# Optimization experiments

Measured on AMD Instinct MI355X. Metric: run time of the kernel, lower is better.

## Reference

```python
import jax, jax.numpy as jnp
import numpy as np
from jax import lax

K = 3          # kernel (patch size)
D = 64         # MPO bond dimension
F = K * K      # feature dim per patch (k^2 * C, C=1)
S = F          # output-index spacing inside each SMPO
OUT = 10       # final output dimension
B = 128        # batch size
H = 81         # image height = width
SIGMA = 1e-3   # 'random_eye' noise scale


def patch_embed(x, k=K):
    """squeeze_image + trigonometric embedding.
    x: (B, h, w) -> unit vectors (B, N, 2) with N=(h/k)*(w/k).
    Each k*k patch row is embedded as the L2-normalized mean of
    [cos(pi/2 x), sin(pi/2 x)] over its k^2 features."""
    b, h, w = x.shape
    p = x.reshape(b, h // k, k, w // k, k).transpose(0, 1, 3, 2, 4)
    p = p.reshape(b, (h // k) * (w // k), k * k)
    ang = 0.5 * jnp.pi * p
    v = jnp.stack([jnp.cos(ang).mean(-1), jnp.sin(ang).mean(-1)], axis=-1)
    return v / jnp.linalg.norm(v, axis=-1, keepdims=True)


def smpo_layer(v, W_out, W_mid):
    """Spaced MPO applied to a product-state MPS, read out per output site.
    v:      (B, n, 2)  input site vectors (n = J*S sites, output at every S-th)
    W_out:  (J, D, D, 2, F)  output-site tensors (identity baseline baked in)
    W_mid:  (J, S-1, D, D, 2) non-output site tensors; effective matrix is
            M = I + einsum('bp,dep->bde', v, W) ('random_eye' init).
    Output row j = L_j . A_j(v) . R_j where L/R are left/right chain
    environments with the other output indices closed with ones.
    Returns (B, J, F)."""
    b, n, _ = v.shape
    J = W_out.shape[0]
    s = n // J
    eye = jnp.eye(D, dtype=v.dtype)
    vg = v.reshape(b, J, s, 2)
    v_out = vg[:, :, 0, :].transpose(1, 0, 2)        # (J, B, 2)
    v_mid = vg[:, :, 1:, :].transpose(1, 2, 0, 3)    # (J, S-1, B, 2)

    def left_step(l, xs):
        A, vo, Wm, vm = xs
        Lj = l                                       # env left of output site j
        l = jnp.einsum('bd,bp,depf->be', l, vo, A)   # Abar (f summed = ones closure)
        for t in range(s - 1):
            M = eye + jnp.einsum('bp,dep->bde', vm[t], Wm[t])
            l = jnp.einsum('bd,bde->be', l, M)
        return l, Lj

    def right_step(r, xs):
        A, vo, Wm, vm = xs
        for t in reversed(range(s - 1)):
            M = eye + jnp.einsum('bp,dep->bde', vm[t], Wm[t])
            r = jnp.einsum('bde,be->bd', M, r)
        Rj = r                                       # env right of output site j
        r = jnp.einsum('bp,depf,be->bd', vo, A, r)
        return r, Rj

    bnd = jnp.zeros((b, D), v.dtype).at[:, 0].set(1.0)  # bond-1 boundary
    xs = (W_out, v_out, W_mid, v_mid)
    _, L = lax.scan(jax.checkpoint(left_step), bnd, xs)
    _, R = lax.scan(jax.checkpoint(right_step), bnd, xs, reverse=True)
    return jnp.einsum('jbd,jdepf,jbp,jbe->bjf', L, W_out, v_out, R)


def final_layer(x, A0, W_mid):
    """Final SMPO (spacing = n, single output index at site 0), fully
    contracted left-to-right. x: (B, n) -> (B, OUT)."""
    ang = 0.5 * jnp.pi * x
    v = jnp.stack([jnp.cos(ang), jnp.sin(ang)], axis=-1)   # (B, n, 2)
    eye = jnp.eye(D, dtype=x.dtype)
    u = jnp.einsum('bp,epo->beo', v[:, 0], A0[0])          # left boundary e0

    def step(u, xs):
        Wm, vm = xs
        M = eye + jnp.einsum('bp,dep->bde', vm, Wm)
        return jnp.einsum('bdo,bde->beo', u, M), None

    u, _ = lax.scan(jax.checkpoint(step), u, (W_mid, v[:, 1:].transpose(1, 0, 2)))
    return u[:, 0, :]                                      # right boundary e0


def setup_inputs() -> dict:
    key = jax.random.key(0)
    ks = jax.random.split(key, 7)
    eyeD = np.eye(D, dtype=np.float32)

    def wout(k, J):  # identity baseline + noise ('random_eye')
        base = jnp.asarray((0.8 / F) * eyeD[:, :, None, None])
        return base + SIGMA * jax.random.normal(k, (J, D, D, 2, F), jnp.float32)

    def wmid(k, J):
        return SIGMA * jax.random.normal(k, (J, S - 1, D, D, 2), jnp.float32)

    x = jax.random.uniform(ks[0], (B, H, H, 1), jnp.float32)
    Wout0 = wout(ks[1], 81)
    Wmid0 = wmid(ks[2], 81)
    Wout1 = wout(ks[3], 9)
    Wmid1 = wmid(ks[4], 9)
    A0f = jnp.asarray(0.1 * eyeD[:, :, None, None]) + SIGMA * jax.random.normal(
        ks[5], (D, D, 2, OUT), jnp.float32)
    WmidF = SIGMA * jax.random.normal(ks[6], (80, D, D, 2), jnp.float32)
    return {"x": x, "Wout0": Wout0, "Wmid0": Wmid0, "Wout1": Wout1,
            "Wmid1": Wmid1, "A0f": A0f, "WmidF": WmidF}


def reference(x, Wout0, Wmid0, Wout1, Wmid1, A0f, WmidF):
    v0 = patch_embed(x[..., 0])                    # (B, 729, 2)
    h1 = smpo_layer(v0, Wout0, Wmid0)              # (B, 81, 9)
    v1 = patch_embed(h1.reshape(-1, 27, 27))       # (B, 81, 2)
    h2 = smpo_layer(v1, Wout1, Wmid1)              # (B, 9, 9)
    return final_layer(h2.reshape(-1, 81), A0f, WmidF)  # (B, 10)
```

## Files before the change

kernel.cpp:

```cpp
#include <hip/hip_runtime.h>
#include <cstdint>
#include <cstddef>


typedef float    f32x16 __attribute__((ext_vector_type(16)));
typedef _Float16 f16x8  __attribute__((ext_vector_type(8)));
typedef __fp16   fp16x2 __attribute__((ext_vector_type(2)));
typedef _Float16 h2_t   __attribute__((ext_vector_type(2)));
typedef const void __attribute__((address_space(1))) gas_t;
typedef void       __attribute__((address_space(3))) las_t;

union U16  { uint4 u; f16x8 h; };
union B16u { uint32_t u[4]; f16x8 h; };
union H2U  { fp16x2 h; uint32_t u; };

__device__ __forceinline__ uint32_t pkf16(float a, float b){
  H2U z; z.h = __builtin_amdgcn_cvt_pkrtz(a, b); return z.u;
}
__device__ __forceinline__ uint32_t pkmul(uint32_t a, uint32_t b){
  H2U x, y, r; x.u = a; y.u = b;
  r.h = x.h * y.h; return r.u;
}
__device__ __forceinline__ uint32_t packh2(float a, float b){
  union { _Float16 h[2]; uint32_t u; } z;
  z.h[0] = (_Float16)a; z.h[1] = (_Float16)b; return z.u;
}
__device__ __forceinline__ float fdot2f(uint32_t wa, uint32_t wb, float acc){
  union U { uint32_t u; h2_t h; };
  U a, b; a.u = wa; b.u = wb;
  return __builtin_amdgcn_fdot2(a.h, b.h, acc, false);
}

#define REC 17408

__global__ void k_build(const float* __restrict__ Wmid, const float* __restrict__ Wout,
                        char* __restrict__ S, int J, int n, int dirR){
  int tid = blockIdx.x*256 + threadIdx.x;
  if (tid >= n*4096) return;
  int gt = tid >> 12, r = tid & 4095;
  int f = r >> 8, ln = (r >> 2) & 63, dw = r & 3;
  int s = f >> 1, m = f & 1;
  int row = m*32 + (ln & 31);
  int kb = s*16 + (ln >> 5)*8 + dw*2;
  int p = kb >> 6, q = kb & 63;
  int jj = gt/9, pos = gt - jj*9;
  int j = dirR ? (J-1-jj) : jj;
  int outs = dirR ? 8 : 0;
  float w[2];
  #pragma unroll
  for (int k2 = 0; k2 < 2; ++k2){
    int qq = q + k2;
    int d = dirR ? row : qq;
    int e = dirR ? qq : row;
    float val;
    if (pos == outs){
      const float* src = Wout + ((((size_t)j*64 + d)*64 + e)*2 + p)*9;
      val = 0.f;
      #pragma unroll
      for (int ff = 0; ff < 9; ++ff) val += src[ff];
      if (d == e) val -= 0.8f;
    } else {
      int mi = dirR ? (7 - pos) : (pos - 1);
      val = Wmid[((((size_t)j*8 + mi)*64 + d)*64 + e)*2 + p];
    }
    w[k2] = val;
  }
  uint32_t* S32 = (uint32_t*)(S + (size_t)gt*REC);
  S32[f*256 + ln*4 + dw] = packh2(w[0]*256.f, w[1]*256.f);
}

__global__ void k_buildF(const float* __restrict__ Wm, char* __restrict__ S){
  int tid = blockIdx.x*256 + threadIdx.x;
  if (tid >= 80*4096) return;
  int gt = tid >> 12, r = tid & 4095;
  int f = r >> 8, ln = (r >> 2) & 63, dw = r & 3;
  int s = f >> 1, m = f & 1;
  int row = m*32 + (ln & 31);
  int kb = s*16 + (ln >> 5)*8 + dw*2;
  int p = kb >> 6, q = kb & 63;
  float w[2];
  #pragma unroll
  for (int k2 = 0; k2 < 2; ++k2){
    int d = q + k2, e = row;
    w[k2] = Wm[(((size_t)gt*64 + d)*64 + e)*2 + p];
  }
  uint32_t* S32 = (uint32_t*)(S + (size_t)gt*REC);
  S32[f*256 + ln*4 + dw] = packh2(w[0]*256.f, w[1]*256.f);
}

__global__ void k_vrec(const float2* __restrict__ v, char* __restrict__ S,
                       int n, int nv, int mode){
  int tid = blockIdx.x*256 + threadIdx.x;
  if (tid >= n*128) return;
  int gt = tid >> 7, b = tid & 127;
  int site = (mode == 0) ? gt : (mode == 1) ? (n-1-gt) : (gt+1);
  *(float2*)(S + (size_t)gt*REC + 16384 + b*8) = v[(size_t)b*nv + site];
}

__global__ void k_embed(const float* __restrict__ img, int Wd, int PG,
                        float2* __restrict__ outv){
  int tid = blockIdx.x*256 + threadIdx.x;
  int NP = PG*PG;
  if (tid >= 128*NP) return;
  int b = tid / NP, s = tid - b*NP;
  int pi = s / PG, pj = s - pi*PG;
  const float* base = img + (size_t)b*Wd*Wd + (size_t)(3*pi)*Wd + 3*pj;
  float cs = 0.f, sn = 0.f;
  #pragma unroll
  for (int r = 0; r < 3; ++r){
    #pragma unroll
    for (int c = 0; c < 3; ++c){
      float x = base[r*Wd + c];
      float s_, c_; sincosf(1.5707963267948966f*x, &s_, &c_);
      cs += c_; sn += s_;
    }
  }
  cs *= (1.f/9.f); sn *= (1.f/9.f);
  float rn = rsqrtf(cs*cs + sn*sn);
  float2 v; v.x = cs*rn; v.y = sn*rn;
  outv[tid] = v;
}

__device__ __forceinline__ void stage17(const char* g, char* l){
  #pragma unroll
  for (int i = 0; i < 17; ++i)
    __builtin_amdgcn_global_load_lds((gas_t*)(const void*)(g + i*1024),
                                     (las_t*)(void*)(l + i*1024), 16, 0, 0);
}

#define MKBASE(acc, bd) do { \
  uint32_t P0 = pkf16(acc[0],acc[1]),  P1 = pkf16(acc[2],acc[3]); \
  uint32_t P2 = pkf16(acc[4],acc[5]),  P3 = pkf16(acc[6],acc[7]); \
  uint32_t Q0 = (uint32_t)__shfl_xor((int)P0, 32); \
  uint32_t Q1 = (uint32_t)__shfl_xor((int)P1, 32); \
  uint32_t Q2 = (uint32_t)__shfl_xor((int)P2, 32); \
  uint32_t Q3 = (uint32_t)__shfl_xor((int)P3, 32); \
  bd[0] = hlo ? P0 : Q2;  bd[1] = hlo ? P1 : Q3; \
  bd[2] = hlo ? Q0 : P2;  bd[3] = hlo ? Q1 : P3; \
  uint32_t R0 = pkf16(acc[8],acc[9]),   R1 = pkf16(acc[10],acc[11]); \
  uint32_t R2 = pkf16(acc[12],acc[13]), R3 = pkf16(acc[14],acc[15]); \
  uint32_t T0 = (uint32_t)__shfl_xor((int)R0, 32); \
  uint32_t T1 = (uint32_t)__shfl_xor((int)R1, 32); \
  uint32_t T2 = (uint32_t)__shfl_xor((int)R2, 32); \
  uint32_t T3 = (uint32_t)__shfl_xor((int)R3, 32); \
  bd[4] = hlo ? R0 : T2;  bd[5] = hlo ? R1 : T3; \
  bd[6] = hlo ? T0 : R2;  bd[7] = hlo ? T1 : R3; \
} while(0)

#define MFMA8(slotp) do { \
  const uint4* fr_ = (const uint4*)(slotp); \
  _Pragma("unroll") \
  for (int s_ = 0; s_ < 8; ++s_){ \
    const int sl_ = s_ & 3; \
    const uint32_t* bb_ = (sl_ < 2) ? bd0 : bd1; \
    const int off_ = (sl_ & 1)*4; \
    const uint32_t scl_ = (s_ < 4) ? px : py; \
    B16u bs_; \
    _Pragma("unroll") \
    for (int dw_ = 0; dw_ < 4; ++dw_) bs_.u[dw_] = pkmul(bb_[off_+dw_], scl_); \
    U16 fa0_, fa1_; \
    fa0_.u = fr_[(2*s_)*64 + ln]; \
    fa1_.u = fr_[(2*s_+1)*64 + ln]; \
    acc0 = __builtin_amdgcn_mfma_f32_32x32x16_f16(fa0_.h, bs_.h, acc0, 0, 0, 0); \
    acc1 = __builtin_amdgcn_mfma_f32_32x32x16_f16(fa1_.h, bs_.h, acc1, 0, 0, 0); \
  } \
} while(0)

#define PROD_SLOOP(buf) do { \
  const uint4* fr = (const uint4*)(buf); \
  _Pragma("unroll") \
  for (int s = 0; s < 8; ++s){ \
    const int sl = s & 3; \
    const uint32_t scl = (s < 4) ? px : py; \
    const int off = (sl & 1)*4; \
    U16 f0, f1; \
    f0.u = fr[(2*s)*64 + ln]; \
    f1.u = fr[(2*s+1)*64 + ln]; \
    { \
      const uint32_t* bb = (sl < 2) ? bl0 : bh0; \
      B16u bs; \
      _Pragma("unroll") \
      for (int dw = 0; dw < 4; ++dw) bs.u[dw] = pkmul(bb[off+dw], scl); \
      a00 = __builtin_amdgcn_mfma_f32_32x32x16_f16(f0.h, bs.h, a00, 0, 0, 0); \
      a10 = __builtin_amdgcn_mfma_f32_32x32x16_f16(f1.h, bs.h, a10, 0, 0, 0); \
    } \
    { \
      const uint32_t* bb = (sl < 2) ? bl1 : bh1; \
      B16u bs; \
      _Pragma("unroll") \
      for (int dw = 0; dw < 4; ++dw) bs.u[dw] = pkmul(bb[off+dw], scl); \
      a01 = __builtin_amdgcn_mfma_f32_32x32x16_f16(f0.h, bs.h, a01, 0, 0, 0); \
      a11 = __builtin_amdgcn_mfma_f32_32x32x16_f16(f1.h, bs.h, a11, 0, 0, 0); \
    } \
  } \
} while(0)

#define PROD_INIT_I() do { \
  _Pragma("unroll") \
  for (int i = 0; i < 16; ++i){ a00[i]=0.f; a01[i]=0.f; a10[i]=0.f; a11[i]=0.f; } \
  if (((i32 >> 2) & 1) == h){ \
    int rr0 = (i32 & 3) | ((i32 >> 3) << 2); \
    _Pragma("unroll") \
    for (int rr = 0; rr < 16; ++rr) \
      if (rr == rr0){ a00[rr] = 1.f; a11[rr] = 1.f; } \
  } \
} while(0)

#define PROD_WRITEOUT(ob, diagc) do { \
  _Pragma("unroll") \
  for (int x = 0; x < 2; ++x){ \
    _Pragma("unroll") \
    for (int y = 0; y < 2; ++y){ \
      const f32x16& A = (x==0) ? (y==0 ? a00 : a01) : (y==0 ? a10 : a11); \
      int C = y*32 + i32; \
      _Pragma("unroll") \
      for (int r = 0; r < 16; ++r){ \
        int R = x*32 + (r & 3) + 8*(r >> 2) + 4*h; \
        float val = (A[r] - ((R == C) ? (diagc) : 0.f))*256.f; \
        float oth = __shfl_xor(val, 1); \
        if (!(ln & 1)){ \
          uint32_t dwv = packh2(val, oth); \
          *(uint32_t*)((ob) + R*128 + ((C*2) ^ ((R & 7) << 4))) = dwv; \
        } \
      } \
    } \
  } \
} while(0)

__global__ __launch_bounds__(512, 1) void k_prod(
    const char* __restrict__ sL, const char* __restrict__ sR,
    const float2* __restrict__ v, char* __restrict__ Tn, char* __restrict__ Wn,
    int J){
  __shared__ __align__(16) char lds[3][16384];
  const int ln = threadIdx.x & 63, w = threadIdx.x >> 6;
  const int wid = (blockIdx.x & 7)*(J*4) + (blockIdx.x >> 3);
  const int bg = wid & 15;
  const int pair = wid >> 4;
  const int dir = pair & 1, j = pair >> 1;
  const int b = bg*8 + w;
  const bool hlo = (ln < 32);
  const int h = ln >> 5, i32 = ln & 31;
  const float INV = 1.f/256.f;
  const char* stream = dir ? sR : sL;
  const int n = J*9;

  float2 vv[9];
  {
    const float2* vbase = v + (size_t)b*n + j*9;
    #pragma unroll
    for (int t = 0; t < 9; ++t) vv[t] = vbase[dir ? (9 - t) : t];
  }
  const float alphaC = (dir && j == J-1) ? 1.0f : 0.8f*(vv[0].x + vv[0].y);
  if (dir && j == J-1){ vv[0].x = 0.f; vv[0].y = 0.f; }

  auto gtf = [&](int t) -> int {
    int g = dir ? ((J-2-j)*9 + 8 + t) : (j*9 + t);
    return g < 0 ? 0 : g;
  };
  auto stage = [&](int t, int sl){
    const char* g0 = stream + (size_t)gtf(t)*REC + (size_t)(2*w)*1024 + (size_t)ln*16;
    __builtin_amdgcn_global_load_lds((gas_t*)(const void*)g0,
                                     (las_t*)(void*)(lds[sl] + 2*w*1024), 16, 0, 0);
    __builtin_amdgcn_global_load_lds((gas_t*)(const void*)(g0 + 1024),
                                     (las_t*)(void*)(lds[sl] + (2*w+1)*1024), 16, 0, 0);
  };

  f32x16 a00, a01, a10, a11;
  PROD_INIT_I();

  stage(0, 0);
  stage(1, 1);
  #pragma unroll
  for (int t = 0; t < 9; ++t){
    asm volatile("s_waitcnt vmcnt(2)" ::: "memory");
    __builtin_amdgcn_s_barrier();
    {
      int tn = (t+2 > 8) ? 8 : (t+2);
      stage(tn, (t+2) % 3);
    }
    uint32_t px = pkf16(vv[t].x*INV, vv[t].x*INV);
    uint32_t py = pkf16(vv[t].y*INV, vv[t].y*INV);
    uint32_t bl0[8], bh0[8], bl1[8], bh1[8];
    MKBASE(a00, bl0); MKBASE(a10, bh0);
    MKBASE(a01, bl1); MKBASE(a11, bh1);
    if (t == 0){
      #pragma unroll
      for (int i = 0; i < 16; ++i){
        a00[i] *= alphaC; a01[i] *= alphaC; a10[i] *= alphaC; a11[i] *= alphaC;
      }
    }
    PROD_SLOOP(lds[t % 3]);
  }

  char* ob = (dir ? Wn : Tn) + ((size_t)b*J + j)*8192;
  PROD_WRITEOUT(ob, alphaC);
}

__global__ __launch_bounds__(512, 1) void k_prodF(
    const char* __restrict__ sF, const float2* __restrict__ vF,
    char* __restrict__ GF){
  __shared__ __align__(16) char lds[3][16384];
  const int ln = threadIdx.x & 63, w = threadIdx.x >> 6;
  const int wid = (blockIdx.x & 7)*20 + (blockIdx.x >> 3);
  const int bg = wid & 15, g = wid >> 4;
  const int b = bg*8 + w;
  const bool hlo = (ln < 32);
  const int h = ln >> 5, i32 = ln & 31;
  const float INV = 1.f/256.f;

  float2 vv[8];
  {
    const float2* vbase = vF + (size_t)b*81 + g*8 + 1;
    #pragma unroll
    for (int t = 0; t < 8; ++t) vv[t] = vbase[t];
  }
  auto stage = [&](int t, int sl){
    const char* g0 = sF + (size_t)(g*8 + t)*REC + (size_t)(2*w)*1024 + (size_t)ln*16;
    __builtin_amdgcn_global_load_lds((gas_t*)(const void*)g0,
                                     (las_t*)(void*)(lds[sl] + 2*w*1024), 16, 0, 0);
    __builtin_amdgcn_global_load_lds((gas_t*)(const void*)(g0 + 1024),
                                     (las_t*)(void*)(lds[sl] + (2*w+1)*1024), 16, 0, 0);
  };

  f32x16 a00, a01, a10, a11;
  PROD_INIT_I();

  stage(0, 0);
  stage(1, 1);
  #pragma unroll
  for (int t = 0; t < 8; ++t){
    asm volatile("s_waitcnt vmcnt(2)" ::: "memory");
    __builtin_amdgcn_s_barrier();
    {
      int tn = (t+2 > 7) ? 7 : (t+2);
      stage(tn, (t+2) % 3);
    }
    uint32_t px = pkf16(vv[t].x*INV, vv[t].x*INV);
    uint32_t py = pkf16(vv[t].y*INV, vv[t].y*INV);
    uint32_t bl0[8], bh0[8], bl1[8], bh1[8];
    MKBASE(a00, bl0); MKBASE(a10, bh0);
    MKBASE(a01, bl1); MKBASE(a11, bh1);
    PROD_SLOOP(lds[t % 3]);
  }

  char* ob = GF + ((size_t)b*10 + g)*8192;
  PROD_WRITEOUT(ob, 1.0f);
}

__global__ __launch_bounds__(64, 1) void k_gscan(
    const char* __restrict__ Tn, const char* __restrict__ Wn,
    const float2* __restrict__ v,
    float* __restrict__ Lout, float* __restrict__ Rout, int J){
  __shared__ __align__(16) char slot[4][8192];
  __shared__ __align__(16) float2 vvs[81];
  __shared__ __align__(16) uint32_t pk32[32];
  const int ln = threadIdx.x;
  const int dir = blockIdx.x >> 7;
  const int b = blockIdx.x & 127;
  const float INV = 1.f/256.f;
  const char* P = (dir ? Wn : Tn) + (size_t)b*J*8192;

  for (int g = ln; g < J; g += 64) vvs[g] = v[(size_t)b*(J*9) + (size_t)g*9];

  auto JD = [&](int g){ return dir ? (J-1-g) : g; };
  auto stage8 = [&](int jx, int sl){
    const char* g0 = P + (size_t)jx*8192 + (size_t)ln*16;
    #pragma unroll
    for (int i = 0; i < 8; ++i)
      __builtin_amdgcn_global_load_lds((gas_t*)(const void*)(g0 + i*1024),
                                       (las_t*)(void*)(slot[sl] + i*1024), 16, 0, 0);
  };

  stage8(JD(0), 0);
  stage8(JD(1 < J-1 ? 1 : J-1), 1);
  stage8(JD(2 < J-1 ? 2 : J-1), 2);

  float st = (ln == 0) ? 1.f : 0.f;
  const uint32_t swz = (uint32_t)(ln & 7) << 4;

  #pragma unroll 1
  for (int g = 0; g < J; ++g){
    const int j = JD(g);
    asm volatile("s_waitcnt vmcnt(16)" ::: "memory");
    if (!dir) Lout[((size_t)j*128 + b)*64 + ln] = st;
    {
      int gn = (g+3 > J-1) ? (J-1) : (g+3);
      stage8(JD(gn), (g+3) & 3);
    }

    float c;
    if (dir) c = (j < J-1) ? 0.8f*(vvs[j+1].x + vvs[j+1].y) : 1.0f;
    else     c = 0.8f*(vvs[j].x + vvs[j].y);

    {
      float o = __shfl_xor(st, 1);
      pk32[ln>>1] = (ln & 1) ? packh2(o, st) : packh2(st, o);
    }
    const char* sp = slot[g & 3] + (size_t)ln*128;
    const uint4* lp = (const uint4*)pk32;
    float acc = 0.f;
    #pragma unroll
    for (int m = 0; m < 8; ++m){
      uint4 q = lp[m];
      uint4 ww = *(const uint4*)(sp + ((m*16) ^ swz));
      acc = fdot2f(ww.x, q.x, acc); acc = fdot2f(ww.y, q.y, acc);
      acc = fdot2f(ww.z, q.z, acc); acc = fdot2f(ww.w, q.w, acc);
    }
    st = c*st + acc*INV;
    if (dir) Rout[((size_t)j*128 + b)*64 + ln] = st;
  }
}

__global__ __launch_bounds__(64, 1) void k_fscan(
    const char* __restrict__ GF, const float* __restrict__ A0f,
    const float2* __restrict__ vF, float* __restrict__ outp){
  __shared__ __align__(16) char slot[4][8192];
  __shared__ __align__(16) uint32_t pk[10][32];
  const int ln = threadIdx.x;
  const int b = blockIdx.x;
  const float INV = 1.f/256.f;
  const char* P = GF + (size_t)b*10*8192;

  float2 v0 = vF[(size_t)b*81];
  float u[10];
  #pragma unroll
  for (int o = 0; o < 10; ++o)
    u[o] = v0.x*A0f[(ln*2+0)*10 + o] + v0.y*A0f[(ln*2+1)*10 + o];

  auto stage8 = [&](int g, int sl){
    const char* g0 = P + (size_t)g*8192 + (size_t)ln*16;
    #pragma unroll
    for (int i = 0; i < 8; ++i)
      __builtin_amdgcn_global_load_lds((gas_t*)(const void*)(g0 + i*1024),
                                       (las_t*)(void*)(slot[sl] + i*1024), 16, 0, 0);
  };

  stage8(0, 0);
  stage8(1, 1);
  stage8(2, 2);
  const uint32_t swz = (uint32_t)(ln & 7) << 4;

  #pragma unroll 1
  for (int g = 0; g < 10; ++g){
    asm volatile("s_waitcnt vmcnt(16)" ::: "memory");
    {
      int gn = (g+3 > 9) ? 9 : (g+3);
      stage8(gn, (g+3) & 3);
    }
    #pragma unroll
    for (int o = 0; o < 10; ++o){
      float ot = __shfl_xor(u[o], 1);
      pk[o][ln>>1] = (ln & 1) ? packh2(ot, u[o]) : packh2(u[o], ot);
    }
    const char* sp = slot[g & 3] + (size_t)ln*128;
    uint4 wr[8];
    #pragma unroll
    for (int m = 0; m < 8; ++m) wr[m] = *(const uint4*)(sp + ((m*16) ^ swz));
    #pragma unroll
    for (int o = 0; o < 10; ++o){
      const uint4* lp = (const uint4*)pk[o];
      float acc = 0.f;
      #pragma unroll
      for (int m = 0; m < 8; ++m){
        uint4 q = lp[m];
        acc = fdot2f(wr[m].x, q.x, acc); acc = fdot2f(wr[m].y, q.y, acc);
        acc = fdot2f(wr[m].z, q.z, acc); acc = fdot2f(wr[m].w, q.w, acc);
      }
      u[o] += acc*INV;
    }
  }
  if (ln == 0){
    #pragma unroll
    for (int o = 0; o < 10; ++o) outp[(size_t)b*10 + o] = u[o];
  }
}

__global__ __launch_bounds__(64, 1) void k_scan_m(
    const char* __restrict__ sL, const char* __restrict__ sR,
    float* __restrict__ Lout, float* __restrict__ Rout, int J, int n){
  __shared__ __align__(16) char lds[4*REC];
  const int ln = threadIdx.x;
  const int wg = blockIdx.x;
  const int dir = wg >> 2;
  const int colbase = (wg & 3)*32;
  const char* stream = dir ? sR : sL;
  float* Sout = dir ? Rout : Lout;
  const int outs = dir ? 8 : 0;
  const int b = colbase + (ln & 31);
  const bool hlo = (ln < 32);
  const int h4 = (ln >> 5)*4;
  const float INV = 1.f/256.f;

  f32x16 acc0, acc1;
  #pragma unroll
  for (int i = 0; i < 16; ++i){ acc0[i] = 0.f; acc1[i] = 0.f; }
  if (hlo) acc0[0] = 1.f;

  const char* gsrc = stream + (size_t)ln*16;
  stage17(gsrc,           lds);
  stage17(gsrc + REC,     lds + REC);
  stage17(gsrc + 2*REC,   lds + 2*REC);

  int pos = 0, jj = 0;
  for (int t = 0; t < n; ++t){
    asm volatile("s_waitcnt vmcnt(34)" ::: "memory");
    const char* slot = lds + (size_t)(t & 3)*REC;
    float2 vv = *(const float2*)(slot + 16384 + b*8);
    int tn = t + 3; if (tn > n-1) tn = n-1;
    stage17(gsrc + (size_t)tn*REC, lds + (size_t)(tn & 3)*REC);

    uint32_t px = pkf16(vv.x*INV, vv.x*INV);
    uint32_t py = pkf16(vv.y*INV, vv.y*INV);
    uint32_t bd0[8], bd1[8];
    MKBASE(acc0, bd0);
    MKBASE(acc1, bd1);

    if (pos == outs){
      int jdx = dir ? (J-1-jj) : jj;
      float* dst = Sout + ((size_t)jdx*128 + b)*64;
      #pragma unroll
      for (int q = 0; q < 4; ++q){
        float4 f0; f0.x = acc0[4*q]; f0.y = acc0[4*q+1]; f0.z = acc0[4*q+2]; f0.w = acc0[4*q+3];
        *(float4*)(dst + 8*q + h4) = f0;
        float4 f1; f1.x = acc1[4*q]; f1.y = acc1[4*q+1]; f1.z = acc1[4*q+2]; f1.w = acc1[4*q+3];
        *(float4*)(dst + 32 + 8*q + h4) = f1;
      }
      float alpha = 0.8f*(vv.x + vv.y);
      #pragma unroll
      for (int i = 0; i < 16; ++i){ acc0[i] *= alpha; acc1[i] *= alpha; }
    }

    MFMA8(slot);

    ++pos; if (pos == 9){ pos = 0; ++jj; }
  }
}

__global__ __launch_bounds__(64, 1) void k_final_m(
    const char* __restrict__ sF, const float* __restrict__ A0f,
    const float2* __restrict__ vF, float* __restrict__ outp){
  __shared__ __align__(16) char lds[4*REC];
  const int ln = threadIdx.x;
  const int wg = blockIdx.x;
  const int o = wg >> 2;
  const int b = (wg & 3)*32 + (ln & 31);
  const bool hlo = (ln < 32);
  const int h4 = (ln >> 5)*4;
  const float INV = 1.f/256.f;

  float2 v0 = vF[(size_t)b*81];
  f32x16 acc0, acc1;
  #pragma unroll
  for (int rg = 0; rg < 16; ++rg){
    int row0 = (rg & 3) + 8*(rg >> 2) + h4;
    acc0[rg] = v0.x*A0f[(row0*2+0)*10 + o] + v0.y*A0f[(row0*2+1)*10 + o];
    int row1 = row0 + 32;
    acc1[rg] = v0.x*A0f[(row1*2+0)*10 + o] + v0.y*A0f[(row1*2+1)*10 + o];
  }
  asm volatile("s_waitcnt vmcnt(0)" ::: "memory");

  const char* gsrc = sF + (size_t)ln*16;
  stage17(gsrc,         lds);
  stage17(gsrc + REC,   lds + REC);
  stage17(gsrc + 2*REC, lds + 2*REC);

  const int n = 80;
  for (int t = 0; t < n; ++t){
    asm volatile("s_waitcnt vmcnt(34)" ::: "memory");
    const char* slot = lds + (size_t)(t & 3)*REC;
    float2 vv = *(const float2*)(slot + 16384 + b*8);
    int tn = t + 3; if (tn > n-1) tn = n-1;
    stage17(gsrc + (size_t)tn*REC, lds + (size_t)(tn & 3)*REC);

    uint32_t px = pkf16(vv.x*INV, vv.x*INV);
    uint32_t py = pkf16(vv.y*INV, vv.y*INV);
    uint32_t bd0[8], bd1[8];
    MKBASE(acc0, bd0);
    MKBASE(acc1, bd1);
    MFMA8(slot);
  }
  if (hlo) outp[(size_t)b*10 + o] = acc0[0];
}

template<bool EMB>
__global__ __launch_bounds__(256) void k_out(
    const float* __restrict__ Wout, const float* __restrict__ Lbuf,
    const float* __restrict__ Rbuf, const float2* __restrict__ v, int n,
    float* __restrict__ hout, float2* __restrict__ vF){
  __shared__ float tile[8][64][20];
  __shared__ float Lsh[32][65];
  const int j = blockIdx.x, bh = blockIdx.y;
  const int q = threadIdx.x >> 5, bl = threadIdx.x & 31;
  const int b = bh*32 + bl;
  for (int idx = threadIdx.x; idx < 32*64; idx += 256){
    int r = idx >> 6, d = idx & 63;
    Lsh[r][d] = Lbuf[((size_t)j*128 + bh*32 + r)*64 + d];
  }
  float Rr[8];
  {
    const float4* Rp = (const float4*)(Rbuf + ((size_t)j*128 + b)*64 + q*8);
    ((float4*)Rr)[0] = Rp[0];
    ((float4*)Rr)[1] = Rp[1];
  }
  float acc[18];
  #pragma unroll
  for (int k = 0; k < 18; ++k) acc[k] = 0.f;
  __syncthreads();
  for (int c = 0; c < 8; ++c){
    #pragma unroll
    for (int k = 0; k < 2; ++k){
      int pi = threadIdx.x*2 + k;
      int d8 = pi >> 6, e = pi & 63;
      const float* src = Wout + ((size_t)(j*64 + c*8 + d8)*64 + e)*18;
      float* dst = &tile[d8][e][0];
      #pragma unroll
      for (int mm = 0; mm < 18; ++mm) dst[mm] = src[mm];
    }
    __syncthreads();
    #pragma unroll 1
    for (int d8 = 0; d8 < 8; ++d8){
      float lw = Lsh[bl][c*8 + d8];
      #pragma unroll
      for (int i = 0; i < 8; ++i){
        int e = q*8 + i;
        float wbe = lw * Rr[i];
        const float* tp = &tile[d8][e][0];
        float4 t0 = *(const float4*)(tp);
        float4 t1 = *(const float4*)(tp+4);
        float4 t2 = *(const float4*)(tp+8);
        float4 t3 = *(const float4*)(tp+12);
        float2 t4 = *(const float2*)(tp+16);
        acc[0]  += wbe*t0.x; acc[1]  += wbe*t0.y; acc[2]  += wbe*t0.z; acc[3]  += wbe*t0.w;
        acc[4]  += wbe*t1.x; acc[5]  += wbe*t1.y; acc[6]  += wbe*t1.z; acc[7]  += wbe*t1.w;
        acc[8]  += wbe*t2.x; acc[9]  += wbe*t2.y; acc[10] += wbe*t2.z; acc[11] += wbe*t2.w;
        acc[12] += wbe*t3.x; acc[13] += wbe*t3.y; acc[14] += wbe*t3.z; acc[15] += wbe*t3.w;
        acc[16] += wbe*t4.x; acc[17] += wbe*t4.y;
      }
    }
    __syncthreads();
  }
  float* red = &tile[0][0][0];
  #pragma unroll
  for (int k = 0; k < 18; ++k) red[((size_t)q*32 + bl)*20 + k] = acc[k];
  __syncthreads();
  if (q == 0){
    float s[18];
    #pragma unroll
    for (int k = 0; k < 18; ++k){
      float t = 0.f;
      #pragma unroll
      for (int g = 0; g < 8; ++g) t += red[((size_t)g*32 + bl)*20 + k];
      s[k] = t;
    }
    float2 vo = v[(size_t)b*n + j*9];
    #pragma unroll
    for (int f = 0; f < 9; ++f){
      float val = vo.x*s[f] + vo.y*s[9+f];
      if (EMB){
        float s_, c_; sincosf(1.5707963267948966f*val, &s_, &c_);
        float2 e2; e2.x = c_; e2.y = s_;
        vF[(size_t)b*81 + j*9 + f] = e2;
      } else {
        hout[(size_t)b*729 + j*9 + f] = val;
      }
    }
  }
}

extern "C" void kernel_launch(void* const* d_in, const int* in_sizes, int n_in,
                              void* d_out, int out_size, void* d_ws, size_t ws_size,
                              hipStream_t stream){
  const float* x     = (const float*)d_in[0];
  const float* Wout0 = (const float*)d_in[1];
  const float* Wmid0 = (const float*)d_in[2];
  const float* Wout1 = (const float*)d_in[3];
  const float* Wmid1 = (const float*)d_in[4];
  const float* A0f   = (const float*)d_in[5];
  const float* WmidF = (const float*)d_in[6];
  float* outp = (float*)d_out;

  char* ws = (char*)d_ws;
  size_t off = 0;
  auto alloc = [&](size_t bytes) -> char* {
    char* p = ws + off;
    off = (off + bytes + 255) & ~(size_t)255;
    return p;
  };
  char* S0L = alloc((size_t)729*REC);
  char* S0R = alloc((size_t)729*REC);
  char* S1L = alloc((size_t)81*REC);
  char* S1R = alloc((size_t)81*REC);
  char* SF  = alloc((size_t)80*REC);
  float2* v0 = (float2*)alloc((size_t)128*729*8);
  float2* v1 = (float2*)alloc((size_t)128*81*8);
  float2* vF = (float2*)alloc((size_t)128*81*8);
  float* L0 = (float*)alloc((size_t)81*128*64*4);
  float* R0 = (float*)alloc((size_t)81*128*64*4);
  float* L1 = (float*)alloc((size_t)9*128*64*4);
  float* R1 = (float*)alloc((size_t)9*128*64*4);
  float* h1 = (float*)alloc((size_t)128*729*4);
  char* Tn1 = alloc((size_t)128*81*8192);
  char* Wn1 = alloc((size_t)128*81*8192);
  size_t need_r7 = off;
  char* Tn2 = alloc((size_t)128*9*8192);
  char* Wn2 = alloc((size_t)128*9*8192);
  char* GF  = alloc((size_t)128*10*8192);
  size_t need_full = off;
  bool full = (ws_size >= need_full);
  bool grp1 = (ws_size >= need_r7);
  (void)in_sizes; (void)n_in; (void)out_size;

  k_build <<<1296,  256, 0, stream>>>(Wmid1, Wout1, S1L, 9, 81, 0);
  k_build <<<1296,  256, 0, stream>>>(Wmid1, Wout1, S1R, 9, 81, 1);
  k_buildF<<<1280,  256, 0, stream>>>(WmidF, SF);
  k_build<<<11664, 256, 0, stream>>>(Wmid0, Wout0, S0L, 81, 729, 0);
  k_build<<<11664, 256, 0, stream>>>(Wmid0, Wout0, S0R, 81, 729, 1);

  k_embed<<<365, 256, 0, stream>>>(x, 81, 27, v0);
  if (grp1){
    k_prod <<<2592, 512, 0, stream>>>(S0L, S0R, v0, Tn1, Wn1, 81);
    k_gscan<<<256, 64, 0, stream>>>(Tn1, Wn1, v0, L0, R0, 81);
  } else {
    k_vrec <<<365, 256, 0, stream>>>(v0, S0L, 729, 729, 0);
    k_vrec <<<365, 256, 0, stream>>>(v0, S0R, 729, 729, 1);
    k_scan_m<<<8, 64, 0, stream>>>(S0L, S0R, L0, R0, 81, 729);
  }
  k_out<false><<<dim3(81,4), 256, 0, stream>>>(Wout0, L0, R0, v0, 729, h1, (float2*)nullptr);

  k_embed<<<41, 256, 0, stream>>>(h1, 27, 9, v1);
  if (full){
    k_prod <<<288, 512, 0, stream>>>(S1L, S1R, v1, Tn2, Wn2, 9);
    k_gscan<<<256, 64, 0, stream>>>(Tn2, Wn2, v1, L1, R1, 9);
  } else {
    k_vrec <<<41, 256, 0, stream>>>(v1, S1L, 81, 81, 0);
    k_vrec <<<41, 256, 0, stream>>>(v1, S1R, 81, 81, 1);
    k_scan_m<<<8, 64, 0, stream>>>(S1L, S1R, L1, R1, 9, 81);
  }
  k_out<true><<<dim3(9,4), 256, 0, stream>>>(Wout1, L1, R1, v1, 81, (float*)nullptr, vF);

  if (full){
    k_prodF<<<160, 512, 0, stream>>>(SF, vF, GF);
    k_fscan<<<128, 64, 0, stream>>>(GF, A0f, vF, outp);
  } else {
    k_vrec <<<40, 256, 0, stream>>>(vF, SF, 80, 81, 2);
    k_final_m<<<40, 64, 0, stream>>>(SF, A0f, vF, outp);
  }
}
```

Measured before the change: 502.2 us.

## Stage all chain steps into LDS up front, with two barriers

Replaces the three-slot rotating LDS ring in k_prod and k_prodF with one LDS slot per step (9 or 8 slots of 16 KB each). The first three steps are loaded and waited on, then the remaining steps are issued in one batch. Compute runs through steps 0-2, then waits once more and finishes the rest. This drops the per-step vmcnt wait and barrier in exchange for up to 144 KB of LDS per block, a long initial wait, and no overlap for the tail loads beyond the first three steps.

```diff
diff --git a/kernel.cpp b/kernel.cpp
--- a/kernel.cpp
+++ b/kernel.cpp
@@ -227,11 +227,26 @@
   } \
 } while(0)
 
+#define PROD_STEP(t, doalpha) do { \
+  uint32_t px = pkf16(vv[t].x*INV, vv[t].x*INV); \
+  uint32_t py = pkf16(vv[t].y*INV, vv[t].y*INV); \
+  uint32_t bl0[8], bh0[8], bl1[8], bh1[8]; \
+  MKBASE(a00, bl0); MKBASE(a10, bh0); \
+  MKBASE(a01, bl1); MKBASE(a11, bh1); \
+  if (doalpha){ \
+    _Pragma("unroll") \
+    for (int i = 0; i < 16; ++i){ \
+      a00[i] *= alphaC; a01[i] *= alphaC; a10[i] *= alphaC; a11[i] *= alphaC; \
+    } \
+  } \
+  PROD_SLOOP(lds + (size_t)(t)*16384); \
+} while(0)
+
 __global__ __launch_bounds__(512, 1) void k_prod(
     const char* __restrict__ sL, const char* __restrict__ sR,
     const float2* __restrict__ v, char* __restrict__ Tn, char* __restrict__ Wn,
     int J){
-  __shared__ __align__(16) char lds[3][16384];
+  __shared__ __align__(16) char lds[9*16384];
   const int ln = threadIdx.x & 63, w = threadIdx.x >> 6;
   const int wid = (blockIdx.x & 7)*(J*4) + (blockIdx.x >> 3);
   const int bg = wid & 15;
@@ -257,40 +272,31 @@
     int g = dir ? ((J-2-j)*9 + 8 + t) : (j*9 + t);
     return g < 0 ? 0 : g;
   };
-  auto stage = [&](int t, int sl){
+  auto stage = [&](int t){
     const char* g0 = stream + (size_t)gtf(t)*REC + (size_t)(2*w)*1024 + (size_t)ln*16;
+    char* l0 = lds + (size_t)t*16384;
     __builtin_amdgcn_global_load_lds((gas_t*)(const void*)g0,
-                                     (las_t*)(void*)(lds[sl] + 2*w*1024), 16, 0, 0);
+                                     (las_t*)(void*)(l0 + 2*w*1024), 16, 0, 0);
     __builtin_amdgcn_global_load_lds((gas_t*)(const void*)(g0 + 1024),
-                                     (las_t*)(void*)(lds[sl] + (2*w+1)*1024), 16, 0, 0);
+                                     (las_t*)(void*)(l0 + (2*w+1)*1024), 16, 0, 0);
   };
 
   f32x16 a00, a01, a10, a11;
   PROD_INIT_I();
 
-  stage(0, 0);
-  stage(1, 1);
-  #pragma unroll
-  for (int t = 0; t < 9; ++t){
-    asm volatile("s_waitcnt vmcnt(2)" ::: "memory");
-    __builtin_amdgcn_s_barrier();
-    {
-      int tn = (t+2 > 8) ? 8 : (t+2);
-      stage(tn, (t+2) % 3);
-    }
-    uint32_t px = pkf16(vv[t].x*INV, vv[t].x*INV);
-    uint32_t py = pkf16(vv[t].y*INV, vv[t].y*INV);
-    uint32_t bl0[8], bh0[8], bl1[8], bh1[8];
-    MKBASE(a00, bl0); MKBASE(a10, bh0);
-    MKBASE(a01, bl1); MKBASE(a11, bh1);
-    if (t == 0){
-      #pragma unroll
-      for (int i = 0; i < 16; ++i){
-        a00[i] *= alphaC; a01[i] *= alphaC; a10[i] *= alphaC; a11[i] *= alphaC;
-      }
-    }
-    PROD_SLOOP(lds[t % 3]);
-  }
+  stage(0); stage(1); stage(2);
+  asm volatile("s_waitcnt vmcnt(0)" ::: "memory");
+  __builtin_amdgcn_s_barrier();
+  #pragma unroll
+  for (int t = 3; t < 9; ++t) stage(t);
+
+  PROD_STEP(0, true);
+  PROD_STEP(1, false);
+  PROD_STEP(2, false);
+  asm volatile("s_waitcnt vmcnt(0)" ::: "memory");
+  __builtin_amdgcn_s_barrier();
+  #pragma unroll
+  for (int t = 3; t < 9; ++t) PROD_STEP(t, false);
 
   char* ob = (dir ? Wn : Tn) + ((size_t)b*J + j)*8192;
   PROD_WRITEOUT(ob, alphaC);
@@ -299,7 +305,7 @@
 __global__ __launch_bounds__(512, 1) void k_prodF(
     const char* __restrict__ sF, const float2* __restrict__ vF,
     char* __restrict__ GF){
-  __shared__ __align__(16) char lds[3][16384];
+  __shared__ __align__(16) char lds[8*16384];
   const int ln = threadIdx.x & 63, w = threadIdx.x >> 6;
   const int wid = (blockIdx.x & 7)*20 + (blockIdx.x >> 3);
   const int bg = wid & 15, g = wid >> 4;
@@ -307,6 +313,7 @@
   const bool hlo = (ln < 32);
   const int h = ln >> 5, i32 = ln & 31;
   const float INV = 1.f/256.f;
+  const float alphaC = 1.0f;
 
   float2 vv[8];
   {
@@ -314,34 +321,31 @@
     #pragma unroll
     for (int t = 0; t < 8; ++t) vv[t] = vbase[t];
   }
-  auto stage = [&](int t, int sl){
+  auto stage = [&](int t){
     const char* g0 = sF + (size_t)(g*8 + t)*REC + (size_t)(2*w)*1024 + (size_t)ln*16;
+    char* l0 = lds + (size_t)t*16384;
     __builtin_amdgcn_global_load_lds((gas_t*)(const void*)g0,
-                                     (las_t*)(void*)(lds[sl] + 2*w*1024), 16, 0, 0);
+                                     (las_t*)(void*)(l0 + 2*w*1024), 16, 0, 0);
     __builtin_amdgcn_global_load_lds((gas_t*)(const void*)(g0 + 1024),
-                                     (las_t*)(void*)(lds[sl] + (2*w+1)*1024), 16, 0, 0);
+                                     (las_t*)(void*)(l0 + (2*w+1)*1024), 16, 0, 0);
   };
 
   f32x16 a00, a01, a10, a11;
   PROD_INIT_I();
 
-  stage(0, 0);
-  stage(1, 1);
-  #pragma unroll
-  for (int t = 0; t < 8; ++t){
-    asm volatile("s_waitcnt vmcnt(2)" ::: "memory");
-    __builtin_amdgcn_s_barrier();
-    {
-      int tn = (t+2 > 7) ? 7 : (t+2);
-      stage(tn, (t+2) % 3);
-    }
-    uint32_t px = pkf16(vv[t].x*INV, vv[t].x*INV);
-    uint32_t py = pkf16(vv[t].y*INV, vv[t].y*INV);
-    uint32_t bl0[8], bh0[8], bl1[8], bh1[8];
-    MKBASE(a00, bl0); MKBASE(a10, bh0);
-    MKBASE(a01, bl1); MKBASE(a11, bh1);
-    PROD_SLOOP(lds[t % 3]);
-  }
+  stage(0); stage(1); stage(2);
+  asm volatile("s_waitcnt vmcnt(0)" ::: "memory");
+  __builtin_amdgcn_s_barrier();
+  #pragma unroll
+  for (int t = 3; t < 8; ++t) stage(t);
+
+  PROD_STEP(0, false);
+  PROD_STEP(1, false);
+  PROD_STEP(2, false);
+  asm volatile("s_waitcnt vmcnt(0)" ::: "memory");
+  __builtin_amdgcn_s_barrier();
+  #pragma unroll
+  for (int t = 3; t < 8; ++t) PROD_STEP(t, false);
 
   char* ob = GF + ((size_t)b*10 + g)*8192;
   PROD_WRITEOUT(ob, 1.0f);
```

Result: slower. 519.7 us (+3.5%).
